# Optimization experiments

Measured on AMD Instinct MI355X. Metric: run time of the kernel, lower is better.

The kernel has to match this reference:

```python
import jax, jax.numpy as jnp
import numpy as np

N = 8192
E = 262144
NFEAT, NHID, NCLASS = 128, 256, 16


def setup_inputs() -> dict:
    key = jax.random.key(0)
    k = jax.random.split(key, 6)
    x = jax.random.normal(k[0], (N, NFEAT), dtype=jnp.float32)
    edge_index = jax.random.randint(k[1], (2, E), 0, N, dtype=jnp.int64)
    edge_weight = jax.random.uniform(k[2], (E,), dtype=jnp.float32)
    W1 = jax.random.normal(k[3], (NFEAT, NHID), dtype=jnp.float32) * (1.0 / np.sqrt(NFEAT))
    b1 = jnp.zeros((NHID,), dtype=jnp.float32)
    W2 = jax.random.normal(k[4], (NHID, NCLASS), dtype=jnp.float32) * (1.0 / np.sqrt(NHID))
    b2 = jnp.zeros((NCLASS,), dtype=jnp.float32)
    return {"x": x, "edge_index": edge_index, "edge_weight": edge_weight,
            "W1": W1, "b1": b1, "W2": W2, "b2": b2}


def _norm_adj(edge_index, edge_weight, num_nodes, dtype):
    # dense scatter-add adjacency (adj[row, col] += w), matching the torch code
    adj = jnp.zeros((num_nodes, num_nodes), dtype=dtype)
    adj = adj.at[edge_index[0], edge_index[1]].add(edge_weight)
    adj = adj + jnp.eye(num_nodes, dtype=dtype)  # self loops
    # degree computed under no_grad in the original -> stop_gradient here
    deg = jax.lax.stop_gradient(jnp.sum(adj, axis=1))
    dinv = jnp.where(deg > 0, deg ** -0.5, jnp.zeros_like(deg))  # inf -> 0
    # D^{-1/2} A D^{-1/2} (diag matmuls expressed as broadcasts, same math)
    return dinv[:, None] * adj * dinv[None, :]


def reference(x, edge_index, edge_weight, W1, b1, W2, b2):
    norm_adj = _norm_adj(edge_index, edge_weight, x.shape[0], x.dtype)
    # submodel: 2-layer GCN, relu(A X W1) -> A H W2 -> log_softmax
    h = jax.nn.relu(norm_adj @ (x @ W1) + b1)
    out = norm_adj @ (h @ W2) + b2
    return jax.nn.log_softmax(out, axis=-1)
```

## Files before the change

kernel.cpp:

```cpp
#include <hip/hip_runtime.h>
#include <math.h>

#define N_NODES 8192
#define N_EDGES 262144
#define NFEAT 128
#define NHID 256
#define NCLASS 16
#define ELLS 96

__device__ inline unsigned int f2bf(float f) {
    unsigned int u = __float_as_uint(f);
    u += 0x7fffu + ((u >> 16) & 1u);
    return u >> 16;
}

#define CVT4(v, f) { \
    f[0] = __uint_as_float((v).x << 16); f[1] = __uint_as_float((v).x & 0xffff0000u); \
    f[2] = __uint_as_float((v).y << 16); f[3] = __uint_as_float((v).y & 0xffff0000u); }

__global__ void zero_kernel(int* __restrict__ p) {
    p[blockIdx.x * 256 + threadIdx.x] = 0;
}

__global__ __launch_bounds__(256) void histscatter_kernel(const int* __restrict__ ei,
                                                          const float* __restrict__ ew,
                                                          int* __restrict__ cnt,
                                                          int2* __restrict__ ell) {
    int e = blockIdx.x * 256 + threadIdx.x;
    int r = ei[e];
    int c = ei[N_EDGES + e];
    float w = ew[e];
    int slot = atomicAdd(&cnt[r], 1);
    ell[r * ELLS + slot] = make_int2(c, __float_as_int(w));
}

__global__ __launch_bounds__(256) void dinvcvt_kernel(const int* __restrict__ cnt,
                                                      const int2* __restrict__ ell,
                                                      const float* __restrict__ x,
                                                      float* __restrict__ dinv,
                                                      uint4* __restrict__ xs) {
    int t = threadIdx.x;
    int j = t & 15;
    int r = blockIdx.x * 16 + (t >> 4);
    int n = cnt[r];
    float sum = 0.0f;
    for (int base = 0; base < n; base += 16) {
        int idx = base + j;
        if (idx < n) sum += __int_as_float(ell[r * ELLS + idx].y);
    }
    #pragma unroll
    for (int off = 1; off < 16; off <<= 1) sum += __shfl_xor(sum, off, 16);
    float di = rsqrtf(sum + 1.0f);
    if (j == 0) dinv[r] = di;
    const float4* xp = (const float4*)(x + (size_t)r * NFEAT + j * 8);
    float4 a = xp[0], b = xp[1];
    uint4 o;
    o.x = f2bf(di * a.x) | (f2bf(di * a.y) << 16);
    o.y = f2bf(di * a.z) | (f2bf(di * a.w) << 16);
    o.z = f2bf(di * b.x) | (f2bf(di * b.y) << 16);
    o.w = f2bf(di * b.z) | (f2bf(di * b.w) << 16);
    xs[r * 16 + j] = o;
}

__global__ __launch_bounds__(256) void layer12_kernel(const int* __restrict__ cnt,
                                                      const int2* __restrict__ ell,
                                                      const uint2* __restrict__ xs2,
                                                      const float* __restrict__ dinv,
                                                      const float* __restrict__ W1,
                                                      const float* __restrict__ b1,
                                                      const float* __restrict__ W2,
                                                      float* __restrict__ V2s) {
    __shared__ float axs[8][NFEAT];
    __shared__ float hs[8][NHID + 4];
    __shared__ float part[256];
    int t = threadIdx.x;

    int lane = t & 31;
    int rloc = t >> 5;
    int r = blockIdx.x * 8 + rloc;
    int n = cnt[r];
    float di = dinv[r];
    uint2 xv = xs2[r * 32 + lane];
    float acc[4];
    CVT4(xv, acc);
    for (int base = 0; base < n; base += 8) {
        int2 cw = ell[r * ELLS + base + (lane & 7)];
        #pragma unroll
        for (int u = 0; u < 8; ++u) {
            int k = base + u;
            int c = __shfl(cw.x, u, 8) & (N_NODES - 1);
            float w = __int_as_float(__shfl(cw.y, u, 8));
            w = (k < n) ? w : 0.0f;
            uint2 v = xs2[c * 32 + lane];
            float vf[4]; CVT4(v, vf);
            #pragma unroll
            for (int i = 0; i < 4; ++i) acc[i] += w * vf[i];
        }
    }
    #pragma unroll
    for (int i = 0; i < 4; ++i) acc[i] *= di;
    ((float4*)&axs[rloc][lane * 4])[0] = make_float4(acc[0], acc[1], acc[2], acc[3]);
    __syncthreads();

    float hacc[8];
    #pragma unroll
    for (int q = 0; q < 8; ++q) hacc[q] = 0.0f;
    #pragma unroll 4
    for (int k = 0; k < NFEAT; ++k) {
        float w = W1[k * NHID + t];
        #pragma unroll
        for (int q = 0; q < 8; ++q) hacc[q] += axs[q][k] * w;
    }
    float bb = b1[t];
    #pragma unroll
    for (int q = 0; q < 8; ++q) {
        float v = hacc[q] + bb;
        hs[q][t] = v > 0.0f ? v : 0.0f;
    }
    __syncthreads();

    int j = t & 15;
    int rq = (t >> 4) & 7;
    int kb = (t >> 7) * 128;
    float p = 0.0f;
    #pragma unroll 8
    for (int k = 0; k < 128; ++k) p += hs[rq][kb + k] * W2[(kb + k) * NCLASS + j];
    part[t] = p;
    __syncthreads();
    if (t < 128) {
        int rg = blockIdx.x * 8 + (t >> 4);
        V2s[rg * NCLASS + (t & 15)] = dinv[rg] * (part[t] + part[t + 128]);
    }
}

__global__ __launch_bounds__(256) void agg2_kernel(const int* __restrict__ cnt,
                                                   const int2* __restrict__ ell,
                                                   const float* __restrict__ V2s,
                                                   const float* __restrict__ dinv,
                                                   const float* __restrict__ b2,
                                                   float* __restrict__ out) {
    int t = threadIdx.x;
    int j = t & 15;
    int r = blockIdx.x * 16 + (t >> 4);
    int n = cnt[r];
    float di = dinv[r];
    float acc = V2s[r * NCLASS + j];
    for (int base = 0; base < n; base += 8) {
        int2 cw = ell[r * ELLS + base + (j & 7)];
        #pragma unroll
        for (int u = 0; u < 8; ++u) {
            int k = base + u;
            int c = __shfl(cw.x, u, 8) & (N_NODES - 1);
            float w = __int_as_float(__shfl(cw.y, u, 8));
            w = (k < n) ? w : 0.0f;
            acc += w * V2s[c * NCLASS + j];
        }
    }
    float v = di * acc + b2[j];
    float mx = v;
    #pragma unroll
    for (int off = 1; off < 16; off <<= 1) mx = fmaxf(mx, __shfl_xor(mx, off));
    float ex = expf(v - mx);
    float ssum = ex;
    #pragma unroll
    for (int off = 1; off < 16; off <<= 1) ssum += __shfl_xor(ssum, off);
    out[r * NCLASS + j] = v - mx - logf(ssum);
}

extern "C" void kernel_launch(void* const* d_in, const int* in_sizes, int n_in,
                              void* d_out, int out_size, void* d_ws, size_t ws_size,
                              hipStream_t stream) {
    const float* x  = (const float*)d_in[0];
    const int*   ei = (const int*)d_in[1];
    const float* ew = (const float*)d_in[2];
    const float* W1 = (const float*)d_in[3];
    const float* b1 = (const float*)d_in[4];
    const float* W2 = (const float*)d_in[5];
    const float* b2 = (const float*)d_in[6];
    float* out = (float*)d_out;

    const int n = N_NODES;

    char* ws = (char*)d_ws;
    int*   cnt  = (int*)  (ws);
    float* dinv = (float*)(ws + 32768);
    int2*  ell  = (int2*) (ws + 65536);
    float* V2s  = (float*)(ws + 8388608);
    uint4* xs   = (uint4*)(ws + 16777216);

    zero_kernel<<<32, 256, 0, stream>>>(cnt);

    histscatter_kernel<<<N_EDGES / 256, 256, 0, stream>>>(ei, ew, cnt, ell);
    dinvcvt_kernel<<<n / 16, 256, 0, stream>>>(cnt, ell, x, dinv, xs);

    layer12_kernel<<<n / 8, 256, 0, stream>>>(cnt, ell, (const uint2*)xs,
                                              dinv, W1, b1, W2, V2s);
    agg2_kernel<<<n / 16, 256, 0, stream>>>(cnt, ell, V2s, dinv, b2, out);
}
```

Baseline: 59.70 us.

## Fuse degree into scatter via atomics and drop bf16 pre-scaled feature pass

Degree sums are now accumulated with float atomics during the edge scatter, which removes the separate dinv/convert kernel. Layer 1 gathers raw fp32 x rows and applies the neighbor normalization per edge, recomputing rsqrt from degree wherever it is needed. This saves one launch and the write and re-read of a bf16 feature copy. In exchange each gathered row is twice as large (fp32 instead of bf16) and the scatter now issues an extra float atomic per edge.

Measured after the change: 69.22 us. 1.16x slower.

```diff
diff --git a/kernel.cpp b/kernel.cpp
--- a/kernel.cpp
+++ b/kernel.cpp
@@ -8,15 +8,6 @@
 #define NCLASS 16
 #define ELLS 96
 
-__device__ inline unsigned int f2bf(float f) {
-    unsigned int u = __float_as_uint(f);
-    u += 0x7fffu + ((u >> 16) & 1u);
-    return u >> 16;
-}
-
-#define CVT4(v, f) { \
-    f[0] = __uint_as_float((v).x << 16); f[1] = __uint_as_float((v).x & 0xffff0000u); \
-    f[2] = __uint_as_float((v).y << 16); f[3] = __uint_as_float((v).y & 0xffff0000u); }
 
 __global__ void zero_kernel(int* __restrict__ p) {
     p[blockIdx.x * 256 + threadIdx.x] = 0;
@@ -24,48 +15,22 @@
 
 __global__ __launch_bounds__(256) void histscatter_kernel(const int* __restrict__ ei,
                                                           const float* __restrict__ ew,
+                                                          float* __restrict__ deg,
                                                           int* __restrict__ cnt,
                                                           int2* __restrict__ ell) {
     int e = blockIdx.x * 256 + threadIdx.x;
     int r = ei[e];
     int c = ei[N_EDGES + e];
     float w = ew[e];
+    atomicAdd(&deg[r], w);
     int slot = atomicAdd(&cnt[r], 1);
     ell[r * ELLS + slot] = make_int2(c, __float_as_int(w));
 }
 
-__global__ __launch_bounds__(256) void dinvcvt_kernel(const int* __restrict__ cnt,
+__global__ __launch_bounds__(256) void layer12_kernel(const float* __restrict__ deg,
+                                                      const int* __restrict__ cnt,
                                                       const int2* __restrict__ ell,
                                                       const float* __restrict__ x,
-                                                      float* __restrict__ dinv,
-                                                      uint4* __restrict__ xs) {
-    int t = threadIdx.x;
-    int j = t & 15;
-    int r = blockIdx.x * 16 + (t >> 4);
-    int n = cnt[r];
-    float sum = 0.0f;
-    for (int base = 0; base < n; base += 16) {
-        int idx = base + j;
-        if (idx < n) sum += __int_as_float(ell[r * ELLS + idx].y);
-    }
-    #pragma unroll
-    for (int off = 1; off < 16; off <<= 1) sum += __shfl_xor(sum, off, 16);
-    float di = rsqrtf(sum + 1.0f);
-    if (j == 0) dinv[r] = di;
-    const float4* xp = (const float4*)(x + (size_t)r * NFEAT + j * 8);
-    float4 a = xp[0], b = xp[1];
-    uint4 o;
-    o.x = f2bf(di * a.x) | (f2bf(di * a.y) << 16);
-    o.y = f2bf(di * a.z) | (f2bf(di * a.w) << 16);
-    o.z = f2bf(di * b.x) | (f2bf(di * b.y) << 16);
-    o.w = f2bf(di * b.z) | (f2bf(di * b.w) << 16);
-    xs[r * 16 + j] = o;
-}
-
-__global__ __launch_bounds__(256) void layer12_kernel(const int* __restrict__ cnt,
-                                                      const int2* __restrict__ ell,
-                                                      const uint2* __restrict__ xs2,
-                                                      const float* __restrict__ dinv,
                                                       const float* __restrict__ W1,
                                                       const float* __restrict__ b1,
                                                       const float* __restrict__ W2,
@@ -79,22 +44,22 @@
     int rloc = t >> 5;
     int r = blockIdx.x * 8 + rloc;
     int n = cnt[r];
-    float di = dinv[r];
-    uint2 xv = xs2[r * 32 + lane];
-    float acc[4];
-    CVT4(xv, acc);
+    float di = rsqrtf(deg[r] + 1.0f);
+    const float4* x4 = (const float4*)x;
+    float4 xv = x4[r * 32 + lane];
+    float acc[4] = {di * xv.x, di * xv.y, di * xv.z, di * xv.w};
     for (int base = 0; base < n; base += 8) {
-        int2 cw = ell[r * ELLS + base + (lane & 7)];
+        int idx = base + (lane & 7);
+        int2 cw = ell[r * ELLS + idx];
+        int cc = cw.x & (N_NODES - 1);
+        float wl = __int_as_float(cw.y) * rsqrtf(deg[cc] + 1.0f);
+        wl = (idx < n) ? wl : 0.0f;
         #pragma unroll
         for (int u = 0; u < 8; ++u) {
-            int k = base + u;
-            int c = __shfl(cw.x, u, 8) & (N_NODES - 1);
-            float w = __int_as_float(__shfl(cw.y, u, 8));
-            w = (k < n) ? w : 0.0f;
-            uint2 v = xs2[c * 32 + lane];
-            float vf[4]; CVT4(v, vf);
-            #pragma unroll
-            for (int i = 0; i < 4; ++i) acc[i] += w * vf[i];
+            int c = __shfl(cc, u, 8);
+            float w = __shfl(wl, u, 8);
+            float4 v = x4[c * 32 + lane];
+            acc[0] += w * v.x; acc[1] += w * v.y; acc[2] += w * v.z; acc[3] += w * v.w;
         }
     }
     #pragma unroll
@@ -129,30 +94,33 @@
     __syncthreads();
     if (t < 128) {
         int rg = blockIdx.x * 8 + (t >> 4);
-        V2s[rg * NCLASS + (t & 15)] = dinv[rg] * (part[t] + part[t + 128]);
+        float dig = rsqrtf(deg[rg] + 1.0f);
+        V2s[rg * NCLASS + (t & 15)] = dig * (part[t] + part[t + 128]);
     }
 }
 
-__global__ __launch_bounds__(256) void agg2_kernel(const int* __restrict__ cnt,
+__global__ __launch_bounds__(256) void agg2_kernel(const float* __restrict__ deg,
+                                                   const int* __restrict__ cnt,
                                                    const int2* __restrict__ ell,
                                                    const float* __restrict__ V2s,
-                                                   const float* __restrict__ dinv,
                                                    const float* __restrict__ b2,
                                                    float* __restrict__ out) {
     int t = threadIdx.x;
     int j = t & 15;
     int r = blockIdx.x * 16 + (t >> 4);
     int n = cnt[r];
-    float di = dinv[r];
+    float di = rsqrtf(deg[r] + 1.0f);
     float acc = V2s[r * NCLASS + j];
     for (int base = 0; base < n; base += 8) {
-        int2 cw = ell[r * ELLS + base + (j & 7)];
+        int idx = base + (j & 7);
+        int2 cw = ell[r * ELLS + idx];
+        int cc = cw.x & (N_NODES - 1);
+        float wl = __int_as_float(cw.y);
+        wl = (idx < n) ? wl : 0.0f;
         #pragma unroll
         for (int u = 0; u < 8; ++u) {
-            int k = base + u;
-            int c = __shfl(cw.x, u, 8) & (N_NODES - 1);
-            float w = __int_as_float(__shfl(cw.y, u, 8));
-            w = (k < n) ? w : 0.0f;
+            int c = __shfl(cc, u, 8);
+            float w = __shfl(wl, u, 8);
             acc += w * V2s[c * NCLASS + j];
         }
     }
@@ -179,21 +147,16 @@
     const float* b2 = (const float*)d_in[6];
     float* out = (float*)d_out;
 
-    const int n = N_NODES;
-
     char* ws = (char*)d_ws;
-    int*   cnt  = (int*)  (ws);
-    float* dinv = (float*)(ws + 32768);
+    float* deg  = (float*)(ws);
+    int*   cnt  = (int*)  (ws + 32768);
     int2*  ell  = (int2*) (ws + 65536);
     float* V2s  = (float*)(ws + 8388608);
-    uint4* xs   = (uint4*)(ws + 16777216);
 
-    zero_kernel<<<32, 256, 0, stream>>>(cnt);
+    zero_kernel<<<64, 256, 0, stream>>>((int*)ws);
 
-    histscatter_kernel<<<N_EDGES / 256, 256, 0, stream>>>(ei, ew, cnt, ell);
-    dinvcvt_kernel<<<n / 16, 256, 0, stream>>>(cnt, ell, x, dinv, xs);
+    histscatter_kernel<<<N_EDGES / 256, 256, 0, stream>>>(ei, ew, deg, cnt, ell);
 
-    layer12_kernel<<<n / 8, 256, 0, stream>>>(cnt, ell, (const uint2*)xs,
-                                              dinv, W1, b1, W2, V2s);
-    agg2_kernel<<<n / 16, 256, 0, stream>>>(cnt, ell, V2s, dinv, b2, out);
+    layer12_kernel<<<N_NODES / 8, 256, 0, stream>>>(deg, cnt, ell, x, W1, b1, W2, V2s);
+    agg2_kernel<<<N_NODES / 16, 256, 0, stream>>>(deg, cnt, ell, V2s, b2, out);
 }
```
